# Optimization experiments

Hardware: AMD Instinct MI355X
Metric: run time of the kernel (lower is better)

## Reference

```python
import jax, jax.numpy as jnp
import numpy as np

N_NODES = 50000

def setup_inputs() -> dict:
    key = jax.random.key(0)
    k1, k2, k3, k4, k5, k6, k7 = jax.random.split(key, 7)
    d_in, d_hid, d_out = 128, 512, 128
    n_edges = 600000
    x = jax.random.normal(k1, (N_NODES, d_in), dtype=jnp.float32)
    edge_index = jax.random.randint(k2, (2, n_edges), 0, N_NODES, dtype=jnp.int64)
    edge_weight = jax.random.uniform(k3, (n_edges,), dtype=jnp.float32)
    # GCNConv params (PyG: weight [in, out], bias [out])
    W1 = jax.random.normal(k4, (d_in, d_hid), dtype=jnp.float32) / np.sqrt(d_in)
    b1 = jax.random.normal(k5, (d_hid,), dtype=jnp.float32) * 0.01
    W2 = jax.random.normal(k6, (d_hid, d_out), dtype=jnp.float32) / np.sqrt(d_hid)
    b2 = jax.random.normal(k7, (d_out,), dtype=jnp.float32) * 0.01
    return {"x": x, "edge_index": edge_index, "edge_weight": edge_weight,
            "W1": W1, "b1": b1, "W2": W2, "b2": b2}

def gcn_conv(x, src, dst, ew, W, b, n_nodes):
    # PyG GCNConv: add self-loops (weight 1), symmetric normalization
    idx = jnp.arange(n_nodes, dtype=src.dtype)
    src_f = jnp.concatenate([src, idx])
    dst_f = jnp.concatenate([dst, idx])
    ew_f = jnp.concatenate([ew, jnp.ones((n_nodes,), dtype=ew.dtype)])
    deg = jax.ops.segment_sum(ew_f, dst_f, num_segments=n_nodes)
    dinv = jnp.where(deg > 0, jax.lax.rsqrt(deg), 0.0)
    norm = dinv[src_f] * ew_f * dinv[dst_f]  # [E+N]
    xw = x @ W  # [N, d_hid]
    msg = xw[src_f] * norm[:, None]  # [E+N, d_hid]
    agg = jax.ops.segment_sum(msg, dst_f, num_segments=n_nodes)
    return agg + b

def reference(x, edge_index, edge_weight, W1, b1, W2, b2):
    src, dst = edge_index[0], edge_index[1]
    h = gcn_conv(x, src, dst, edge_weight, W1, b1, N_NODES)
    h = jax.nn.relu(h)
    out = jax.nn.relu(h @ W2 + b2)
    return out
```

## Files before the change

### kernel.cpp

```cpp
#include <hip/hip_runtime.h>
#include <math.h>


typedef __attribute__((ext_vector_type(8))) short short8v;
typedef __attribute__((ext_vector_type(4))) float floatx4;

__device__ __forceinline__ short f2bf(float f) {
    unsigned u = __builtin_bit_cast(unsigned, f);
    unsigned r = (u + 0x7FFFu + ((u >> 16) & 1u)) >> 16;
    return (short)r;
}
__device__ __forceinline__ float bf2f(short s) {
    return __builtin_bit_cast(float, ((unsigned)(unsigned short)s) << 16);
}

__global__ __launch_bounds__(256) void k_initprep(int* __restrict__ counts,
                                                  float* __restrict__ deg, int n,
                                                  const float* __restrict__ W1,
                                                  const float* __restrict__ W2,
                                                  short* __restrict__ W1t,
                                                  short* __restrict__ W2t) {
    int i = blockIdx.x * 256 + threadIdx.x;
    if (i < n) { counts[i] = 0; deg[i] = 1.0f; }
    if (i < 65536) {
        int c = i >> 7, k = i & 127;
        W1t[i] = f2bf(W1[k * 512 + c]);
    } else if (i < 131072) {
        int j = i - 65536;
        int c = j >> 9, k = j & 511;
        W2t[j] = f2bf(W2[k * 128 + c]);
    }
}

__global__ __launch_bounds__(256) void k_hist(const int* __restrict__ dst,
                                              const float* __restrict__ ew,
                                              int* __restrict__ counts,
                                              float* __restrict__ deg, int E) {
    int e = blockIdx.x * 256 + threadIdx.x;
    if (e < E) {
        int d = dst[e];
        atomicAdd(&counts[d], 1);
        atomicAdd(&deg[d], ew[e]);
    }
}

__global__ __launch_bounds__(256) void k_scanA(const int* __restrict__ counts,
                                               int* __restrict__ offsets,
                                               int* __restrict__ blockSum,
                                               float* __restrict__ deg, int n) {
    __shared__ int sdata[256];
    const int tid = threadIdx.x;
    const int i = blockIdx.x * 256 + tid;
    int c = (i < n) ? counts[i] : 0;
    sdata[tid] = c;
    __syncthreads();
#pragma unroll
    for (int off = 1; off < 256; off <<= 1) {
        int t = (tid >= off) ? sdata[tid - off] : 0;
        __syncthreads();
        sdata[tid] += t;
        __syncthreads();
    }
    if (i < n) offsets[i] = sdata[tid] - c;
    if (tid == 255) blockSum[blockIdx.x] = sdata[255];
    if (i < n) {
        float d = deg[i];
        deg[i] = (d > 0.f) ? rsqrtf(d) : 0.f;
    }
}

__global__ __launch_bounds__(256) void k_scanB(int* __restrict__ blockSum, int nb) {
    __shared__ int sdata[256];
    const int tid = threadIdx.x;
    int v = (tid < nb) ? blockSum[tid] : 0;
    sdata[tid] = v;
    __syncthreads();
#pragma unroll
    for (int off = 1; off < 256; off <<= 1) {
        int t = (tid >= off) ? sdata[tid - off] : 0;
        __syncthreads();
        sdata[tid] += t;
        __syncthreads();
    }
    if (tid < nb) blockSum[tid] = sdata[tid] - v;
}

__global__ __launch_bounds__(256) void k_scanC(int* __restrict__ offsets,
                                               const int* __restrict__ blockSum, int n) {
    const int i = blockIdx.x * 256 + threadIdx.x;
    if (i < n) offsets[i] += blockSum[blockIdx.x];
}

__global__ __launch_bounds__(256) void k_scatter(const int* __restrict__ src,
                                                 const int* __restrict__ dst,
                                                 const float* __restrict__ ew,
                                                 const float* __restrict__ dinv,
                                                 int* __restrict__ offsets,
                                                 int2* __restrict__ sedge, int E) {
    int e = blockIdx.x * 256 + threadIdx.x;
    if (e >= E) return;
    int s = src[e];
    int d = dst[e];
    float coef = dinv[s] * ew[e] * dinv[d];
    int pos = atomicAdd(&offsets[d], 1);
    sedge[pos] = make_int2(s, __builtin_bit_cast(int, coef));
}

__global__ __launch_bounds__(256) void k_gmlp(const int* __restrict__ offsets,
                                              const int* __restrict__ counts,
                                              const int2* __restrict__ sedge,
                                              const float* __restrict__ dinv,
                                              const float* __restrict__ x,
                                              const short* __restrict__ W1t,
                                              const float* __restrict__ b1,
                                              const short* __restrict__ W2t,
                                              const float* __restrict__ b2,
                                              float* __restrict__ out, int n) {
    __shared__ __align__(16) short yhi[32 * 128];
    __shared__ __align__(16) short ylo[32 * 128];
    __shared__ __align__(16) short hlds[32 * 512];
    const int tid  = threadIdx.x;
    const int wave = tid >> 6;
    const int lane = tid & 63;
    const int l15  = lane & 15;
    const int lg   = lane >> 4;
    const int row0 = blockIdx.x * 32;
    const float2* x2 = (const float2*)x;

    for (int i = 0; i < 8; ++i) {
        const int r = wave * 8 + i;
        const int node = row0 + r;
        float2 acc = make_float2(0.f, 0.f);
        if (node < n) {
            int o1 = offsets[node];
            int o0 = o1 - counts[node];
            float di = dinv[node];
            float2 xv = x2[(size_t)node * 64 + lane];
            acc.x = di * di * xv.x;
            acc.y = di * di * xv.y;
            int j = o0;
            for (; j + 4 <= o1; j += 4) {
                int2 e0 = sedge[j], e1 = sedge[j + 1], e2 = sedge[j + 2], e3 = sedge[j + 3];
                float2 v0 = x2[(size_t)e0.x * 64 + lane];
                float2 v1 = x2[(size_t)e1.x * 64 + lane];
                float2 v2 = x2[(size_t)e2.x * 64 + lane];
                float2 v3 = x2[(size_t)e3.x * 64 + lane];
                float c0 = __builtin_bit_cast(float, e0.y);
                float c1 = __builtin_bit_cast(float, e1.y);
                float c2 = __builtin_bit_cast(float, e2.y);
                float c3 = __builtin_bit_cast(float, e3.y);
                acc.x = fmaf(c0, v0.x, acc.x); acc.y = fmaf(c0, v0.y, acc.y);
                acc.x = fmaf(c1, v1.x, acc.x); acc.y = fmaf(c1, v1.y, acc.y);
                acc.x = fmaf(c2, v2.x, acc.x); acc.y = fmaf(c2, v2.y, acc.y);
                acc.x = fmaf(c3, v3.x, acc.x); acc.y = fmaf(c3, v3.y, acc.y);
            }
            for (; j < o1; ++j) {
                int2 e = sedge[j];
                float2 v = x2[(size_t)e.x * 64 + lane];
                float c = __builtin_bit_cast(float, e.y);
                acc.x = fmaf(c, v.x, acc.x);
                acc.y = fmaf(c, v.y, acc.y);
            }
        }
        short hx = f2bf(acc.x);
        short hy = f2bf(acc.y);
        short lx = f2bf(acc.x - bf2f(hx));
        short ly = f2bf(acc.y - bf2f(hy));
        const int e = (2 * lane) ^ ((r & 7) << 3);
        *(short2*)&yhi[r * 128 + e] = make_short2(hx, hy);
        *(short2*)&ylo[r * 128 + e] = make_short2(lx, ly);
    }
    __syncthreads();

    const int cb1 = wave * 128;
    floatx4 acc[2][8];
#pragma unroll
    for (int m = 0; m < 2; ++m)
#pragma unroll
        for (int nn = 0; nn < 8; ++nn) acc[m][nn] = (floatx4)0.0f;

#pragma unroll
    for (int kk = 0; kk < 4; ++kk) {
        const int k0 = kk * 32 + lg * 8;
        short8v bf[8];
#pragma unroll
        for (int nn = 0; nn < 8; ++nn)
            bf[nn] = *(const short8v*)(W1t + (size_t)(cb1 + nn * 16 + l15) * 128 + k0);
#pragma unroll
        for (int m = 0; m < 2; ++m) {
            const int r = m * 16 + l15;
            const int ke = k0 ^ ((r & 7) << 3);
            short8v ahi = *(const short8v*)&yhi[r * 128 + ke];
            short8v alo = *(const short8v*)&ylo[r * 128 + ke];
#pragma unroll
            for (int nn = 0; nn < 8; ++nn)
                acc[m][nn] = __builtin_amdgcn_mfma_f32_16x16x32_bf16(ahi, bf[nn], acc[m][nn], 0, 0, 0);
#pragma unroll
            for (int nn = 0; nn < 8; ++nn)
                acc[m][nn] = __builtin_amdgcn_mfma_f32_16x16x32_bf16(alo, bf[nn], acc[m][nn], 0, 0, 0);
        }
    }

#pragma unroll
    for (int m = 0; m < 2; ++m)
#pragma unroll
        for (int nn = 0; nn < 8; ++nn) {
            const int c = cb1 + nn * 16 + l15;
            const float bb = b1[c];
#pragma unroll
            for (int i = 0; i < 4; ++i) {
                const int r = m * 16 + lg * 4 + i;
                float v = acc[m][nn][i] + bb;
                v = v > 0.f ? v : 0.f;
                hlds[r * 512 + (c ^ ((r & 7) << 3))] = f2bf(v);
            }
        }
    __syncthreads();

    const int cb2 = wave * 32;
    floatx4 acc2[2][2];
#pragma unroll
    for (int m = 0; m < 2; ++m)
#pragma unroll
        for (int nn = 0; nn < 2; ++nn) acc2[m][nn] = (floatx4)0.0f;

#pragma unroll
    for (int kk = 0; kk < 16; ++kk) {
        const int k0 = kk * 32 + lg * 8;
        short8v bf2[2];
#pragma unroll
        for (int nn = 0; nn < 2; ++nn)
            bf2[nn] = *(const short8v*)(W2t + (size_t)(cb2 + nn * 16 + l15) * 512 + k0);
#pragma unroll
        for (int m = 0; m < 2; ++m) {
            const int r = m * 16 + l15;
            short8v a = *(const short8v*)&hlds[r * 512 + (k0 ^ ((r & 7) << 3))];
#pragma unroll
            for (int nn = 0; nn < 2; ++nn)
                acc2[m][nn] = __builtin_amdgcn_mfma_f32_16x16x32_bf16(a, bf2[nn], acc2[m][nn], 0, 0, 0);
        }
    }

#pragma unroll
    for (int m = 0; m < 2; ++m)
#pragma unroll
        for (int nn = 0; nn < 2; ++nn) {
            const int c = cb2 + nn * 16 + l15;
            const float bb = b2[c];
#pragma unroll
            for (int i = 0; i < 4; ++i) {
                const int rg = row0 + m * 16 + lg * 4 + i;
                if (rg < n) {
                    float v = acc2[m][nn][i] + bb;
                    out[(size_t)rg * 128 + c] = v > 0.f ? v : 0.f;
                }
            }
        }
}

extern "C" void kernel_launch(void* const* d_in, const int* in_sizes, int n_in,
                              void* d_out, int out_size, void* d_ws, size_t ws_size,
                              hipStream_t stream) {
    const float* x  = (const float*)d_in[0];
    const int*   ei = (const int*)d_in[1];
    const float* ew = (const float*)d_in[2];
    const float* W1 = (const float*)d_in[3];
    const float* b1 = (const float*)d_in[4];
    const float* W2 = (const float*)d_in[5];
    const float* b2 = (const float*)d_in[6];
    float* out = (float*)d_out;

    const int N = in_sizes[0] / 128;
    const int E = in_sizes[2];
    const int* src = ei;
    const int* dst = ei + E;
    const int NB = (N + 255) / 256;

    float* deg      = (float*)d_ws;
    int*   counts   = (int*)(deg + N);
    int*   offsets  = counts + N;
    int*   blockSum = offsets + N;
    int2*  sedge    = (int2*)((((uintptr_t)(blockSum + 256)) + 15) & ~(uintptr_t)15);
    short* W1t      = (short*)(sedge + E);
    short* W2t      = W1t + 65536;

    int nb;
    k_initprep<<<512, 256, 0, stream>>>(counts, deg, N, W1, W2, W1t, W2t);
    nb = (E + 255) / 256;
    k_hist<<<nb, 256, 0, stream>>>(dst, ew, counts, deg, E);
    k_scanA<<<NB, 256, 0, stream>>>(counts, offsets, blockSum, deg, N);
    k_scanB<<<1, 256, 0, stream>>>(blockSum, NB);
    k_scanC<<<NB, 256, 0, stream>>>(offsets, blockSum, N);
    nb = (E + 255) / 256;
    k_scatter<<<nb, 256, 0, stream>>>(src, dst, ew, deg, offsets, sedge, E);
    nb = (N + 31) / 32;
    k_gmlp<<<nb, 256, 0, stream>>>(offsets, counts, sedge, deg, x,
                                   W1t, b1, W2t, b2, out, N);
}
```

Baseline: 316.5 us.

## Gather from bf16 copy of x and split gather and MLP into separate kernels

Converts x to bf16 in the init kernel so the edge gather reads half the bytes per neighbour row. Splits the fused gather+MLP kernel into a one-wave-per-node gather kernel that writes a bf16 aggregate to global memory, followed by an MFMA MLP kernel that reads it directly. It also drops the hi/lo split compensation, halving the first-layer MFMA work. Precision drops because both inputs and aggregates are rounded to bf16. An extra kernel launch and a global round trip for the aggregate are added. The ybf buffer is read for padded rows up to a multiple of 32 that are never written.

```diff
diff --git a/kernel.cpp b/kernel.cpp
--- a/kernel.cpp
+++ b/kernel.cpp
@@ -10,8 +10,11 @@
     unsigned r = (u + 0x7FFFu + ((u >> 16) & 1u)) >> 16;
     return (short)r;
 }
-__device__ __forceinline__ float bf2f(short s) {
-    return __builtin_bit_cast(float, ((unsigned)(unsigned short)s) << 16);
+__device__ __forceinline__ float bfu_lo(unsigned u) {
+    return __builtin_bit_cast(float, u << 16);
+}
+__device__ __forceinline__ float bfu_hi(unsigned u) {
+    return __builtin_bit_cast(float, u & 0xFFFF0000u);
 }
 
 __global__ __launch_bounds__(256) void k_initprep(int* __restrict__ counts,
@@ -19,8 +22,17 @@
                                                   const float* __restrict__ W1,
                                                   const float* __restrict__ W2,
                                                   short* __restrict__ W1t,
-                                                  short* __restrict__ W2t) {
+                                                  short* __restrict__ W2t,
+                                                  const float* __restrict__ x,
+                                                  short* __restrict__ xbf) {
     int i = blockIdx.x * 256 + threadIdx.x;
+    int nx4 = n * 32;
+    if (i < nx4) {
+        float4 v = ((const float4*)x)[i];
+        short4 s;
+        s.x = f2bf(v.x); s.y = f2bf(v.y); s.z = f2bf(v.z); s.w = f2bf(v.w);
+        *(short4*)&xbf[(size_t)i * 4] = s;
+    }
     if (i < n) { counts[i] = 0; deg[i] = 1.0f; }
     if (i < 65536) {
         int c = i >> 7, k = i & 127;
@@ -106,18 +118,56 @@
     sedge[pos] = make_int2(s, __builtin_bit_cast(int, coef));
 }
 
-__global__ __launch_bounds__(256) void k_gmlp(const int* __restrict__ offsets,
-                                              const int* __restrict__ counts,
-                                              const int2* __restrict__ sedge,
-                                              const float* __restrict__ dinv,
-                                              const float* __restrict__ x,
-                                              const short* __restrict__ W1t,
-                                              const float* __restrict__ b1,
-                                              const short* __restrict__ W2t,
-                                              const float* __restrict__ b2,
-                                              float* __restrict__ out, int n) {
-    __shared__ __align__(16) short yhi[32 * 128];
-    __shared__ __align__(16) short ylo[32 * 128];
+__global__ __launch_bounds__(256) void k_gather(const int* __restrict__ offsets,
+                                                const int* __restrict__ counts,
+                                                const int2* __restrict__ sedge,
+                                                const float* __restrict__ dinv,
+                                                const unsigned* __restrict__ xbf_u,
+                                                unsigned* __restrict__ ybf_u, int n) {
+    int wid = (blockIdx.x * 256 + threadIdx.x) >> 6;
+    if (wid >= n) return;
+    int lane = threadIdx.x & 63;
+    int o1 = offsets[wid];
+    int o0 = o1 - counts[wid];
+    float di = dinv[wid];
+    unsigned xs = xbf_u[(size_t)wid * 64 + lane];
+    float2 acc;
+    acc.x = di * di * bfu_lo(xs);
+    acc.y = di * di * bfu_hi(xs);
+    int j = o0;
+    for (; j + 4 <= o1; j += 4) {
+        int2 e0 = sedge[j], e1 = sedge[j + 1], e2 = sedge[j + 2], e3 = sedge[j + 3];
+        unsigned v0 = xbf_u[(size_t)e0.x * 64 + lane];
+        unsigned v1 = xbf_u[(size_t)e1.x * 64 + lane];
+        unsigned v2 = xbf_u[(size_t)e2.x * 64 + lane];
+        unsigned v3 = xbf_u[(size_t)e3.x * 64 + lane];
+        float c0 = __builtin_bit_cast(float, e0.y);
+        float c1 = __builtin_bit_cast(float, e1.y);
+        float c2 = __builtin_bit_cast(float, e2.y);
+        float c3 = __builtin_bit_cast(float, e3.y);
+        acc.x = fmaf(c0, bfu_lo(v0), acc.x); acc.y = fmaf(c0, bfu_hi(v0), acc.y);
+        acc.x = fmaf(c1, bfu_lo(v1), acc.x); acc.y = fmaf(c1, bfu_hi(v1), acc.y);
+        acc.x = fmaf(c2, bfu_lo(v2), acc.x); acc.y = fmaf(c2, bfu_hi(v2), acc.y);
+        acc.x = fmaf(c3, bfu_lo(v3), acc.x); acc.y = fmaf(c3, bfu_hi(v3), acc.y);
+    }
+    for (; j < o1; ++j) {
+        int2 e = sedge[j];
+        unsigned v = xbf_u[(size_t)e.x * 64 + lane];
+        float c = __builtin_bit_cast(float, e.y);
+        acc.x = fmaf(c, bfu_lo(v), acc.x);
+        acc.y = fmaf(c, bfu_hi(v), acc.y);
+    }
+    unsigned lo = (unsigned)(unsigned short)f2bf(acc.x);
+    unsigned hi = (unsigned)(unsigned short)f2bf(acc.y);
+    ybf_u[(size_t)wid * 64 + lane] = lo | (hi << 16);
+}
+
+__global__ __launch_bounds__(256) void k_mlp(const short* __restrict__ ybf,
+                                             const short* __restrict__ W1t,
+                                             const float* __restrict__ b1,
+                                             const short* __restrict__ W2t,
+                                             const float* __restrict__ b2,
+                                             float* __restrict__ out, int n) {
     __shared__ __align__(16) short hlds[32 * 512];
     const int tid  = threadIdx.x;
     const int wave = tid >> 6;
@@ -125,52 +175,6 @@
     const int l15  = lane & 15;
     const int lg   = lane >> 4;
     const int row0 = blockIdx.x * 32;
-    const float2* x2 = (const float2*)x;
-
-    for (int i = 0; i < 8; ++i) {
-        const int r = wave * 8 + i;
-        const int node = row0 + r;
-        float2 acc = make_float2(0.f, 0.f);
-        if (node < n) {
-            int o1 = offsets[node];
-            int o0 = o1 - counts[node];
-            float di = dinv[node];
-            float2 xv = x2[(size_t)node * 64 + lane];
-            acc.x = di * di * xv.x;
-            acc.y = di * di * xv.y;
-            int j = o0;
-            for (; j + 4 <= o1; j += 4) {
-                int2 e0 = sedge[j], e1 = sedge[j + 1], e2 = sedge[j + 2], e3 = sedge[j + 3];
-                float2 v0 = x2[(size_t)e0.x * 64 + lane];
-                float2 v1 = x2[(size_t)e1.x * 64 + lane];
-                float2 v2 = x2[(size_t)e2.x * 64 + lane];
-                float2 v3 = x2[(size_t)e3.x * 64 + lane];
-                float c0 = __builtin_bit_cast(float, e0.y);
-                float c1 = __builtin_bit_cast(float, e1.y);
-                float c2 = __builtin_bit_cast(float, e2.y);
-                float c3 = __builtin_bit_cast(float, e3.y);
-                acc.x = fmaf(c0, v0.x, acc.x); acc.y = fmaf(c0, v0.y, acc.y);
-                acc.x = fmaf(c1, v1.x, acc.x); acc.y = fmaf(c1, v1.y, acc.y);
-                acc.x = fmaf(c2, v2.x, acc.x); acc.y = fmaf(c2, v2.y, acc.y);
-                acc.x = fmaf(c3, v3.x, acc.x); acc.y = fmaf(c3, v3.y, acc.y);
-            }
-            for (; j < o1; ++j) {
-                int2 e = sedge[j];
-                float2 v = x2[(size_t)e.x * 64 + lane];
-                float c = __builtin_bit_cast(float, e.y);
-                acc.x = fmaf(c, v.x, acc.x);
-                acc.y = fmaf(c, v.y, acc.y);
-            }
-        }
-        short hx = f2bf(acc.x);
-        short hy = f2bf(acc.y);
-        short lx = f2bf(acc.x - bf2f(hx));
-        short ly = f2bf(acc.y - bf2f(hy));
-        const int e = (2 * lane) ^ ((r & 7) << 3);
-        *(short2*)&yhi[r * 128 + e] = make_short2(hx, hy);
-        *(short2*)&ylo[r * 128 + e] = make_short2(lx, ly);
-    }
-    __syncthreads();
 
     const int cb1 = wave * 128;
     floatx4 acc[2][8];
@@ -188,16 +192,10 @@
             bf[nn] = *(const short8v*)(W1t + (size_t)(cb1 + nn * 16 + l15) * 128 + k0);
 #pragma unroll
         for (int m = 0; m < 2; ++m) {
-            const int r = m * 16 + l15;
-            const int ke = k0 ^ ((r & 7) << 3);
-            short8v ahi = *(const short8v*)&yhi[r * 128 + ke];
-            short8v alo = *(const short8v*)&ylo[r * 128 + ke];
+            short8v a = *(const short8v*)(ybf + (size_t)(row0 + m * 16 + l15) * 128 + k0);
 #pragma unroll
             for (int nn = 0; nn < 8; ++nn)
-                acc[m][nn] = __builtin_amdgcn_mfma_f32_16x16x32_bf16(ahi, bf[nn], acc[m][nn], 0, 0, 0);
-#pragma unroll
-            for (int nn = 0; nn < 8; ++nn)
-                acc[m][nn] = __builtin_amdgcn_mfma_f32_16x16x32_bf16(alo, bf[nn], acc[m][nn], 0, 0, 0);
+                acc[m][nn] = __builtin_amdgcn_mfma_f32_16x16x32_bf16(a, bf[nn], acc[m][nn], 0, 0, 0);
         }
     }
 
@@ -275,6 +273,8 @@
     const int* src = ei;
     const int* dst = ei + E;
     const int NB = (N + 255) / 256;
+    const int NBM = (N + 31) / 32;
+    const int NROWS = NBM * 32;
 
     float* deg      = (float*)d_ws;
     int*   counts   = (int*)(deg + N);
@@ -283,9 +283,12 @@
     int2*  sedge    = (int2*)((((uintptr_t)(blockSum + 256)) + 15) & ~(uintptr_t)15);
     short* W1t      = (short*)(sedge + E);
     short* W2t      = W1t + 65536;
+    short* xbf      = (short*)((((uintptr_t)(W2t + 65536)) + 15) & ~(uintptr_t)15);
+    short* ybf      = xbf + (size_t)N * 128;
 
     int nb;
-    k_initprep<<<512, 256, 0, stream>>>(counts, deg, N, W1, W2, W1t, W2t);
+    nb = (N * 32 + 255) / 256;
+    k_initprep<<<nb, 256, 0, stream>>>(counts, deg, N, W1, W2, W1t, W2t, x, xbf);
     nb = (E + 255) / 256;
     k_hist<<<nb, 256, 0, stream>>>(dst, ew, counts, deg, E);
     k_scanA<<<NB, 256, 0, stream>>>(counts, offsets, blockSum, deg, N);
@@ -293,7 +296,8 @@
     k_scanC<<<NB, 256, 0, stream>>>(offsets, blockSum, N);
     nb = (E + 255) / 256;
     k_scatter<<<nb, 256, 0, stream>>>(src, dst, ew, deg, offsets, sedge, E);
-    nb = (N + 31) / 32;
-    k_gmlp<<<nb, 256, 0, stream>>>(offsets, counts, sedge, deg, x,
-                                   W1t, b1, W2t, b2, out, N);
-}
+    nb = (N * 64 + 255) / 256;
+    k_gather<<<nb, 256, 0, stream>>>(offsets, counts, sedge, deg,
+                                     (const unsigned*)xbf, (unsigned*)ybf, N);
+    k_mlp<<<NBM, 256, 0, stream>>>(ybf, W1t, b1, W2t, b2, out, N);
+}
```

Measured after the change: 283.9 us. -10.3%, faster.
